# Performance work log

Hardware: AMD Instinct MI355X
Metric: run time of the kernel (lower is better)

## Reference

```python
import jax, jax.numpy as jnp
import numpy as np

T, B, H = 512, 32, 512   # seq, batch, hidden_dim (hidden has 2*H channels)
D = 512                  # label_dim
V = 32000                # vocab
L = 2048                 # number of labels (spans)
K = 2                    # tags per label (regularized ragged tags)


def setup_inputs() -> dict:
    key = jax.random.key(0)
    ks = jax.random.split(key, 11)
    hidden = jax.random.normal(ks[0], (T, B, 2 * H), dtype=jnp.float32)
    begins = jax.random.randint(ks[1], (L,), 1, T - 1)   # begin-1 >= 0
    ends = jax.random.randint(ks[2], (L,), 1, T - 1)     # end <= T-1, end-1 >= 0
    bids = jax.random.randint(ks[3], (L,), 0, B)
    tags = jax.random.randint(ks[4], (L, K), 0, V)
    s = 1.0 / np.sqrt(2 * H)
    Wc = jax.random.uniform(ks[5], (D, 2 * H), minval=-s, maxval=s, dtype=jnp.float32)
    bc = jax.random.uniform(ks[6], (D,), minval=-s, maxval=s, dtype=jnp.float32)
    Wp = jax.random.uniform(ks[7], (D, 2 * H), minval=-s, maxval=s, dtype=jnp.float32)
    bp = jax.random.uniform(ks[8], (D,), minval=-s, maxval=s, dtype=jnp.float32)
    s2 = 1.0 / np.sqrt(D)
    Wo = jax.random.uniform(ks[9], (V, D), minval=-s2, maxval=s2, dtype=jnp.float32)
    bo = jnp.zeros((V,), jnp.float32)
    # discard probs per SoftmaxLoss._discard_probs from synthetic counts
    counts = jax.random.uniform(ks[10], (V,), minval=0.5, maxval=100.0, dtype=jnp.float32)
    freqs = counts / counts.sum()
    discard_probs = jnp.maximum(1.0 - jnp.sqrt(1e-4 / freqs), 0.0)
    return dict(hidden=hidden, Wc=Wc, bc=bc, Wp=Wp, bp=bp, Wo=Wo, bo=bo,
                discard_probs=discard_probs, begins=begins, ends=ends,
                bids=bids, tags=tags)


def reference(hidden, Wc, bc, Wp, bp, Wo, bo, discard_probs,
              begins, ends, bids, tags):
    Hd = hidden.shape[-1] // 2
    # span gathers (vectorized over all labels)
    h_bm1 = hidden[begins - 1, bids]                 # [L, 2H]
    h_end = hidden[ends, bids]                       # [L, 2H]
    context = jnp.concatenate([h_bm1[:, :Hd], h_end[:, Hd:]], axis=-1)  # [L, 2H]
    phrase = (hidden[begins, bids] + hidden[ends - 1, bids]) * 0.5      # [L, 2H]
    # FFNs (dropout = identity in eval mode)
    cf = jnp.tanh(context @ Wc.T + bc)               # [L, D]
    pf = jnp.tanh(phrase @ Wp.T + bp)                # [L, D]
    feats = jnp.concatenate([cf, pf], axis=0)        # [2L, D]
    # softmax loss with discard-prob scaling
    logsm = jax.nn.log_softmax(feats @ Wo.T + bo, axis=-1)  # [2L, V]
    tg = jnp.concatenate([tags, tags], axis=0)       # [2L, K]
    neg = -jnp.take_along_axis(logsm, tg, axis=-1)   # [2L, K]
    ratio = 1.0 - discard_probs[tg]                  # [2L, K]
    loss_rows = (neg * ratio).sum(-1) / ratio.sum(-1)  # [2L]
    n = tg.shape[0]
    return (loss_rows.sum() / (n + 1e-5)).reshape(1)
```

## Files before the change

kernel.cpp:

```cpp
#include <hip/hip_runtime.h>
#include <stdint.h>

typedef uint16_t u16;
typedef uint8_t  u8;
typedef __bf16 bf16x8 __attribute__((ext_vector_type(8)));
typedef float f32x4 __attribute__((ext_vector_type(4)));
typedef int i32x4 __attribute__((ext_vector_type(4)));
typedef int i32x8 __attribute__((ext_vector_type(8)));

#define NSC    16
#define NTILES 250
#define NPART  (2 * NSC)
#define NROWS  4096

__device__ __forceinline__ u16 f2b(float x) {
    uint32_t u = __float_as_uint(x);
    u += 0x7FFF + ((u >> 16) & 1);
    return (u16)(u >> 16);
}

__device__ __forceinline__ u8 f32_to_fp8(float x) {
    uint32_t sign = (__float_as_uint(x) >> 24) & 0x80;
    float ax = fminf(fabsf(x), 448.f);
    uint32_t r;
    if (ax < 0.015625f) {
        r = (uint32_t)(int)rintf(ax * 512.f);
    } else {
        uint32_t u = __float_as_uint(ax);
        u += 0x0007FFFF + ((u >> 20) & 1);
        r = (((u >> 23) - 120) << 3) | ((u >> 20) & 7);
    }
    return (u8)(sign | r);
}

__device__ __forceinline__ float fp8_val(int b) {
    int e = (b >> 3) & 0xF, m = b & 7;
    float v = e ? __uint_as_float((uint32_t)(((e + 120) << 23) | (m << 20)))
                : (float)m * 0.001953125f;
    return (b & 0x80) ? -v : v;
}

__device__ __forceinline__ void cp16(const void* g, void* l) {
    __builtin_amdgcn_global_load_lds(
        (const __attribute__((address_space(1))) uint32_t*)g,
        (__attribute__((address_space(3))) uint32_t*)l, 16, 0, 0);
}

__device__ __forceinline__ float fast_tanh(float x) {
    x = fminf(15.f, fmaxf(-15.f, x));
    float e = __expf(2.f * x);
    return (e - 1.f) / (e + 1.f);
}

__global__ void k_convert8(const float* __restrict__ src, u8* __restrict__ dst, int n) {
    int i = (blockIdx.x * blockDim.x + threadIdx.x) * 4;
    int stride = gridDim.x * blockDim.x * 4;
    for (; i < n; i += stride) {
        float4 v = *(const float4*)(src + i);
        u8 o[4] = {f32_to_fp8(v.x * 32.f), f32_to_fp8(v.y * 32.f),
                   f32_to_fp8(v.z * 32.f), f32_to_fp8(v.w * 32.f)};
        *(uint32_t*)(dst + i) = *(const uint32_t*)o;
    }
}

__global__ void k_prep(const float* __restrict__ Wc, const float* __restrict__ Wp,
                       const float* __restrict__ hidden, const int* __restrict__ begins,
                       const int* __restrict__ ends, const int* __restrict__ bids,
                       u16* __restrict__ Wc_b, u16* __restrict__ Wp_b,
                       u16* __restrict__ ctx, u16* __restrict__ phr) {
    int b = blockIdx.x;
    if (b < 256) {
        int i = b * 2048 + threadIdx.x * 8;
        float4 a0 = *(const float4*)(Wc + i), a1 = *(const float4*)(Wc + i + 4);
        float4 p0 = *(const float4*)(Wp + i), p1 = *(const float4*)(Wp + i + 4);
        u16 oc[8] = {f2b(a0.x), f2b(a0.y), f2b(a0.z), f2b(a0.w),
                     f2b(a1.x), f2b(a1.y), f2b(a1.z), f2b(a1.w)};
        u16 op[8] = {f2b(p0.x), f2b(p0.y), f2b(p0.z), f2b(p0.w),
                     f2b(p1.x), f2b(p1.y), f2b(p1.z), f2b(p1.w)};
        *(int4*)(Wc_b + i) = *(const int4*)oc;
        *(int4*)(Wp_b + i) = *(const int4*)op;
        return;
    }
    int l = b - 256;
    int bg = begins[l], e = ends[l], bd = bids[l];
    const float* h_bm1 = hidden + ((size_t)(bg - 1) * 32 + bd) * 1024;
    const float* h_e   = hidden + ((size_t)e * 32 + bd) * 1024;
    const float* h_b   = hidden + ((size_t)bg * 32 + bd) * 1024;
    const float* h_em1 = hidden + ((size_t)(e - 1) * 32 + bd) * 1024;
    int d = threadIdx.x * 4;
    float4 c4 = (d < 512) ? *(const float4*)(h_bm1 + d) : *(const float4*)(h_e + d);
    float4 b4 = *(const float4*)(h_b + d);
    float4 e4 = *(const float4*)(h_em1 + d);
    u16 co[4] = {f2b(c4.x), f2b(c4.y), f2b(c4.z), f2b(c4.w)};
    u16 po[4] = {f2b(0.5f * (b4.x + e4.x)), f2b(0.5f * (b4.y + e4.y)),
                 f2b(0.5f * (b4.z + e4.z)), f2b(0.5f * (b4.w + e4.w))};
    *(uint64_t*)(ctx + (size_t)l * 1024 + d) = *(const uint64_t*)co;
    *(uint64_t*)(phr + (size_t)l * 1024 + d) = *(const uint64_t*)po;
}

__global__ __launch_bounds__(256) void k_feats(const u16* __restrict__ ctx, const u16* __restrict__ phr,
        const u16* __restrict__ Wc, const u16* __restrict__ Wp,
        const float* __restrict__ bc, const float* __restrict__ bp,
        u8* __restrict__ feats) {
    __shared__ __align__(16) u16 lA[64 * 32];
    __shared__ __align__(16) u16 lB[64 * 32];
    int z = blockIdx.z;
    const u16* A = z ? phr : ctx;
    const u16* W = z ? Wp : Wc;
    const float* bias = z ? bp : bc;
    int m0 = blockIdx.x * 64;
    int n0 = blockIdx.y * 64;
    int t = threadIdx.x;
    int lane = t & 63, w = t >> 6;
    int lrow = lane & 15, lq = lane >> 4;
    f32x4 zero = {0.f, 0.f, 0.f, 0.f};
    f32x4 acc[4];
    for (int i = 0; i < 4; i++) acc[i] = zero;
    int row = t >> 2, kseg = (t & 3) * 8;
    for (int kt = 0; kt < 32; kt++) {
        int k0 = kt * 32;
        __syncthreads();
        cp16(&A[(size_t)(m0 + row) * 1024 + k0 + kseg], &lA[t * 8]);
        cp16(&W[(size_t)(n0 + row) * 1024 + k0 + kseg], &lB[t * 8]);
        __syncthreads();
        bf16x8 af = *(bf16x8*)&lA[(w * 16 + lrow) * 32 + lq * 8];
        for (int ns = 0; ns < 4; ns++) {
            bf16x8 bfr = *(bf16x8*)&lB[(ns * 16 + lrow) * 32 + lq * 8];
            acc[ns] = __builtin_amdgcn_mfma_f32_16x16x32_bf16(af, bfr, acc[ns], 0, 0, 0);
        }
    }
    int zbase = z * 2048;
    for (int ns = 0; ns < 4; ns++) {
        int col = n0 + ns * 16 + lrow;
        float bv = bias[col];
        for (int r = 0; r < 4; r++) {
            int orow = zbase + m0 + w * 16 + lq * 4 + r;
            feats[(size_t)orow * 512 + col] = f32_to_fp8(16.f * fast_tanh(acc[ns][r] + bv));
        }
    }
}

__global__ __launch_bounds__(256, 2) void k_lse(const u8* __restrict__ feats,
        const u8* __restrict__ Wo, const float* __restrict__ bo, float* __restrict__ ps) {
    __shared__ __align__(16) u8 lds[4][128 * 128];
    int m0 = blockIdx.x * 128;
    int sc = blockIdx.y;
    int ts = (NTILES * sc) / NSC, te = (NTILES * (sc + 1)) / NSC;
    int t = threadIdx.x;
    int lane = t & 63, w = t >> 6;
    int lrow = lane & 15, lq = lane >> 4;
    int wrow = (w & 1) * 64, wcol = (w >> 1) * 64;
    int xm = lrow & 7;
    int xoA = ((2 * lq) ^ xm) * 16;
    int xoB = ((2 * lq + 1) ^ xm) * 16;

    int srow = t >> 3;
    int kb = ((t & 7) ^ ((t >> 3) & 7)) * 16;

    i32x8 af[4][4];
#pragma unroll
    for (int mi = 0; mi < 4; mi++)
#pragma unroll
        for (int kc = 0; kc < 4; kc++) {
            const u8* pa = feats + (size_t)(m0 + wrow + mi * 16 + lrow) * 512
                         + kc * 128 + lq * 32;
            i32x4 lo = *(const i32x4*)pa;
            i32x4 hi = *(const i32x4*)(pa + 16);
            af[mi][kc] = __builtin_shufflevector(lo, hi, 0, 1, 2, 3, 4, 5, 6, 7);
        }

    auto stageB = [&](int slot, int gr) {
        const u8* pB = Wo + (size_t)((gr >> 2) * 128 + srow) * 512 + (gr & 3) * 128 + kb;
        for (int j = 0; j < 4; j++)
            cp16(pB + (size_t)(32 * j) * 512, &lds[slot][t * 16 + j * 4096]);
    };

    float s_state[4][4];
    for (int mi = 0; mi < 4; mi++)
        for (int r = 0; r < 4; r++) s_state[mi][r] = 0.f;
    f32x4 zero = {0.f, 0.f, 0.f, 0.f};
    f32x4 acc[4][4];
    const float inv512 = 1.f / 512.f;

    int gr0 = ts * 4;
    stageB(0, gr0);
    stageB(1, gr0 + 1);
    stageB(2, gr0 + 2);

    for (int tile = ts; tile < te; ++tile) {
        int grt = tile * 4;
        bool notlast = (tile + 1 < te);
#pragma unroll
        for (int mi = 0; mi < 4; mi++)
#pragma unroll
            for (int ni = 0; ni < 4; ni++) acc[mi][ni] = zero;
#pragma unroll
        for (int kc = 0; kc < 4; kc++) {
            if (notlast || kc < 2)
                asm volatile("s_waitcnt vmcnt(8)" ::: "memory");
            else if (kc == 2)
                asm volatile("s_waitcnt vmcnt(4)" ::: "memory");
            else
                asm volatile("s_waitcnt vmcnt(0)" ::: "memory");
            __builtin_amdgcn_s_barrier();
            if (notlast || kc == 0)
                stageB((kc + 3) & 3, grt + kc + 3);
            const u8* bufB = lds[kc];
            __builtin_amdgcn_s_setprio(1);
#pragma unroll
            for (int ni = 0; ni < 4; ni++) {
                const u8* pb = bufB + (wcol + ni * 16 + lrow) * 128;
                i32x4 blo = *(const i32x4*)(pb + xoA);
                i32x4 bhi = *(const i32x4*)(pb + xoB);
                i32x8 bfr = __builtin_shufflevector(blo, bhi, 0, 1, 2, 3, 4, 5, 6, 7);
#pragma unroll
                for (int mi = 0; mi < 4; mi++)
                    acc[mi][ni] = __builtin_amdgcn_mfma_scale_f32_16x16x128_f8f6f4(
                        af[mi][kc], bfr, acc[mi][ni], 0, 0,
                        0, 0x7F7F7F7F, 0, 0x7F7F7F7F);
            }
            __builtin_amdgcn_s_setprio(0);
        }
        int n0 = tile * 128;
#pragma unroll
        for (int ni = 0; ni < 4; ni++) {
            float bv = bo[n0 + wcol + ni * 16 + lrow];
#pragma unroll
            for (int mi = 0; mi < 4; mi++)
#pragma unroll
                for (int r = 0; r < 4; r++)
                    s_state[mi][r] += __expf(fmaf(acc[mi][ni][r], inv512, bv));
        }
    }
    for (int mi = 0; mi < 4; mi++)
    for (int r = 0; r < 4; r++) {
        float s = s_state[mi][r];
        for (int off = 1; off < 16; off <<= 1) s += __shfl_xor(s, off);
        if (lrow == 0) {
            int row = m0 + wrow + mi * 16 + lq * 4 + r;
            ps[row * NPART + sc * 2 + (w >> 1)] = s;
        }
    }
}

__global__ void k_taglog(const u8* __restrict__ feats, const u8* __restrict__ Wo,
        const float* __restrict__ bo, const int* __restrict__ tags, float* __restrict__ tlog) {
    int i = blockIdx.x * 4 + (threadIdx.x >> 6);
    int lane = threadIdx.x & 63;
    int t0 = tags[(i & 2047) * 2 + 0];
    int t1 = tags[(i & 2047) * 2 + 1];
    uint64_t fa = *(const uint64_t*)(feats + (size_t)i * 512 + lane * 8);
    uint64_t wa = *(const uint64_t*)(Wo + (size_t)t0 * 512 + lane * 8);
    uint64_t wb = *(const uint64_t*)(Wo + (size_t)t1 * 512 + lane * 8);
    float s0 = 0.f, s1 = 0.f;
    for (int j = 0; j < 8; j++) {
        float fv = fp8_val((int)((fa >> (8 * j)) & 0xFF));
        s0 += fv * fp8_val((int)((wa >> (8 * j)) & 0xFF));
        s1 += fv * fp8_val((int)((wb >> (8 * j)) & 0xFF));
    }
    for (int off = 32; off >= 1; off >>= 1) {
        s0 += __shfl_down(s0, off);
        s1 += __shfl_down(s1, off);
    }
    if (lane == 0) {
        tlog[i * 2 + 0] = s0 * (1.f / 512.f) + bo[t0];
        tlog[i * 2 + 1] = s1 * (1.f / 512.f) + bo[t1];
    }
}

__global__ void k_final(const float* __restrict__ ps,
        const float* __restrict__ tlog, const int* __restrict__ tags,
        const float* __restrict__ dp, float* __restrict__ out) {
    __shared__ float red[256];
    int i = blockIdx.x * 256 + threadIdx.x;
    float S = 0.f;
    for (int j = 0; j < NPART; j++) S += ps[i * NPART + j];
    float lse = logf(S);
    float num = 0.f, den = 0.f;
    for (int k = 0; k < 2; k++) {
        int tg = tags[(i & 2047) * 2 + k];
        float r = 1.0f - dp[tg];
        num += r * (lse - tlog[i * 2 + k]);
        den += r;
    }
    red[threadIdx.x] = num / den;
    __syncthreads();
    for (int s = 128; s > 0; s >>= 1) {
        if (threadIdx.x < s) red[threadIdx.x] += red[threadIdx.x + s];
        __syncthreads();
    }
    if (threadIdx.x == 0) atomicAdd(out, red[0] / (4096.0f + 1e-5f));
}

extern "C" void kernel_launch(void* const* d_in, const int* in_sizes, int n_in,
                              void* d_out, int out_size, void* d_ws, size_t ws_size,
                              hipStream_t stream) {
    const float* hidden = (const float*)d_in[0];
    const float* Wc     = (const float*)d_in[1];
    const float* bc     = (const float*)d_in[2];
    const float* Wp     = (const float*)d_in[3];
    const float* bp     = (const float*)d_in[4];
    const float* Wo     = (const float*)d_in[5];
    const float* bo     = (const float*)d_in[6];
    const float* dp     = (const float*)d_in[7];
    const int* begins   = (const int*)d_in[8];
    const int* ends     = (const int*)d_in[9];
    const int* bids     = (const int*)d_in[10];
    const int* tags     = (const int*)d_in[11];
    float* out = (float*)d_out;

    u8*  Wo8     = (u8*)d_ws;
    u16* Wc_b    = (u16*)((char*)d_ws + 16384000);
    u16* Wp_b    = Wc_b + 524288;
    u16* ctx_b   = Wp_b + 524288;
    u16* phr_b   = ctx_b + 2097152;
    u8*  feats8  = (u8*)(phr_b + 2097152);
    float* ps    = (float*)ctx_b;
    float* tlog  = ps + NROWS * NPART;

    k_convert8<<<2048, 256, 0, stream>>>(Wo, Wo8, 16384000);
    k_prep<<<2304, 256, 0, stream>>>(Wc, Wp, hidden, begins, ends, bids,
                                     Wc_b, Wp_b, ctx_b, phr_b);
    k_feats<<<dim3(32, 8, 2), 256, 0, stream>>>(ctx_b, phr_b, Wc_b, Wp_b, bc, bp, feats8);
    k_lse<<<dim3(32, NSC), 256, 0, stream>>>(feats8, Wo8, bo, ps);
    k_taglog<<<1024, 256, 0, stream>>>(feats8, Wo8, bo, tags, tlog);
    hipMemsetAsync(d_out, 0, sizeof(float), stream);
    k_final<<<16, 256, 0, stream>>>(ps, tlog, tags, dp, out);
}
```

Baseline: 279.0 us.

## Restructure LSE kernel to 8 waves each owning 16 rows across all columns

The LSE GEMM block grows from 4 to 8 waves (512 threads). Each wave now computes a 16-row strip across all 128 columns of the tile, instead of a 64x64 quadrant. This cuts per-wave accumulator and A-fragment registers and halves per-thread staging loads, aiming for higher occupancy and latency hiding. The cost is that each B fragment read from LDS feeds only one MFMA instead of four, so LDS read traffic per MFMA rises. The partial-sum layout drops from 2*NSC to NSC per row to match.

Result: slower. 782.3 us (+180.4%).

```diff
diff --git a/kernel.cpp b/kernel.cpp
--- a/kernel.cpp
+++ b/kernel.cpp
@@ -10,7 +10,7 @@
 
 #define NSC    16
 #define NTILES 250
-#define NPART  (2 * NSC)
+#define NPART  NSC
 #define NROWS  4096
 
 __device__ __forceinline__ u16 f2b(float x) {
@@ -140,7 +140,7 @@
     }
 }
 
-__global__ __launch_bounds__(256, 2) void k_lse(const u8* __restrict__ feats,
+__global__ __launch_bounds__(512, 4) void k_lse(const u8* __restrict__ feats,
         const u8* __restrict__ Wo, const float* __restrict__ bo, float* __restrict__ ps) {
     __shared__ __align__(16) u8 lds[4][128 * 128];
     int m0 = blockIdx.x * 128;
@@ -149,7 +149,6 @@
     int t = threadIdx.x;
     int lane = t & 63, w = t >> 6;
     int lrow = lane & 15, lq = lane >> 4;
-    int wrow = (w & 1) * 64, wcol = (w >> 1) * 64;
     int xm = lrow & 7;
     int xoA = ((2 * lq) ^ xm) * 16;
     int xoB = ((2 * lq + 1) ^ xm) * 16;
@@ -157,29 +156,26 @@
     int srow = t >> 3;
     int kb = ((t & 7) ^ ((t >> 3) & 7)) * 16;
 
-    i32x8 af[4][4];
-#pragma unroll
-    for (int mi = 0; mi < 4; mi++)
+    i32x8 af[4];
+    {
+        const u8* pa = feats + (size_t)(m0 + w * 16 + lrow) * 512 + lq * 32;
 #pragma unroll
         for (int kc = 0; kc < 4; kc++) {
-            const u8* pa = feats + (size_t)(m0 + wrow + mi * 16 + lrow) * 512
-                         + kc * 128 + lq * 32;
-            i32x4 lo = *(const i32x4*)pa;
-            i32x4 hi = *(const i32x4*)(pa + 16);
-            af[mi][kc] = __builtin_shufflevector(lo, hi, 0, 1, 2, 3, 4, 5, 6, 7);
-        }
+            i32x4 lo = *(const i32x4*)(pa + kc * 128);
+            i32x4 hi = *(const i32x4*)(pa + kc * 128 + 16);
+            af[kc] = __builtin_shufflevector(lo, hi, 0, 1, 2, 3, 4, 5, 6, 7);
+        }
+    }
 
     auto stageB = [&](int slot, int gr) {
         const u8* pB = Wo + (size_t)((gr >> 2) * 128 + srow) * 512 + (gr & 3) * 128 + kb;
-        for (int j = 0; j < 4; j++)
-            cp16(pB + (size_t)(32 * j) * 512, &lds[slot][t * 16 + j * 4096]);
+        cp16(pB, &lds[slot][t * 16]);
+        cp16(pB + (size_t)64 * 512, &lds[slot][t * 16 + 8192]);
     };
 
-    float s_state[4][4];
-    for (int mi = 0; mi < 4; mi++)
-        for (int r = 0; r < 4; r++) s_state[mi][r] = 0.f;
+    float s_state[4] = {0.f, 0.f, 0.f, 0.f};
     f32x4 zero = {0.f, 0.f, 0.f, 0.f};
-    f32x4 acc[4][4];
+    f32x4 acc[8];
     const float inv512 = 1.f / 512.f;
 
     int gr0 = ts * 4;
@@ -191,15 +187,13 @@
         int grt = tile * 4;
         bool notlast = (tile + 1 < te);
 #pragma unroll
-        for (int mi = 0; mi < 4; mi++)
-#pragma unroll
-            for (int ni = 0; ni < 4; ni++) acc[mi][ni] = zero;
+        for (int ni = 0; ni < 8; ni++) acc[ni] = zero;
 #pragma unroll
         for (int kc = 0; kc < 4; kc++) {
             if (notlast || kc < 2)
-                asm volatile("s_waitcnt vmcnt(8)" ::: "memory");
+                asm volatile("s_waitcnt vmcnt(4)" ::: "memory");
             else if (kc == 2)
-                asm volatile("s_waitcnt vmcnt(4)" ::: "memory");
+                asm volatile("s_waitcnt vmcnt(2)" ::: "memory");
             else
                 asm volatile("s_waitcnt vmcnt(0)" ::: "memory");
             __builtin_amdgcn_s_barrier();
@@ -208,37 +202,32 @@
             const u8* bufB = lds[kc];
             __builtin_amdgcn_s_setprio(1);
 #pragma unroll
-            for (int ni = 0; ni < 4; ni++) {
-                const u8* pb = bufB + (wcol + ni * 16 + lrow) * 128;
+            for (int ni = 0; ni < 8; ni++) {
+                const u8* pb = bufB + (ni * 16 + lrow) * 128;
                 i32x4 blo = *(const i32x4*)(pb + xoA);
                 i32x4 bhi = *(const i32x4*)(pb + xoB);
                 i32x8 bfr = __builtin_shufflevector(blo, bhi, 0, 1, 2, 3, 4, 5, 6, 7);
-#pragma unroll
-                for (int mi = 0; mi < 4; mi++)
-                    acc[mi][ni] = __builtin_amdgcn_mfma_scale_f32_16x16x128_f8f6f4(
-                        af[mi][kc], bfr, acc[mi][ni], 0, 0,
-                        0, 0x7F7F7F7F, 0, 0x7F7F7F7F);
+                acc[ni] = __builtin_amdgcn_mfma_scale_f32_16x16x128_f8f6f4(
+                    af[kc], bfr, acc[ni], 0, 0,
+                    0, 0x7F7F7F7F, 0, 0x7F7F7F7F);
             }
             __builtin_amdgcn_s_setprio(0);
         }
         int n0 = tile * 128;
 #pragma unroll
-        for (int ni = 0; ni < 4; ni++) {
-            float bv = bo[n0 + wcol + ni * 16 + lrow];
-#pragma unroll
-            for (int mi = 0; mi < 4; mi++)
-#pragma unroll
-                for (int r = 0; r < 4; r++)
-                    s_state[mi][r] += __expf(fmaf(acc[mi][ni][r], inv512, bv));
-        }
-    }
-    for (int mi = 0; mi < 4; mi++)
+        for (int ni = 0; ni < 8; ni++) {
+            float bv = bo[n0 + ni * 16 + lrow];
+#pragma unroll
+            for (int r = 0; r < 4; r++)
+                s_state[r] += __expf(fmaf(acc[ni][r], inv512, bv));
+        }
+    }
     for (int r = 0; r < 4; r++) {
-        float s = s_state[mi][r];
+        float s = s_state[r];
         for (int off = 1; off < 16; off <<= 1) s += __shfl_xor(s, off);
         if (lrow == 0) {
-            int row = m0 + wrow + mi * 16 + lq * 4 + r;
-            ps[row * NPART + sc * 2 + (w >> 1)] = s;
+            int row = m0 + w * 16 + lq * 4 + r;
+            ps[row * NPART + sc] = s;
         }
     }
 }
@@ -322,7 +311,7 @@
     k_prep<<<2304, 256, 0, stream>>>(Wc, Wp, hidden, begins, ends, bids,
                                      Wc_b, Wp_b, ctx_b, phr_b);
     k_feats<<<dim3(32, 8, 2), 256, 0, stream>>>(ctx_b, phr_b, Wc_b, Wp_b, bc, bp, feats8);
-    k_lse<<<dim3(32, NSC), 256, 0, stream>>>(feats8, Wo8, bo, ps);
+    k_lse<<<dim3(32, NSC), 512, 0, stream>>>(feats8, Wo8, bo, ps);
     k_taglog<<<1024, 256, 0, stream>>>(feats8, Wo8, bo, tags, tlog);
     hipMemsetAsync(d_out, 0, sizeof(float), stream);
     k_final<<<16, 256, 0, stream>>>(ps, tlog, tags, dp, out);
```

## Fuse Wo fp8 conversion into prep kernel and widen LSE blocks to 512 threads

Applied to the files above, without the earlier changes.

Folds the Wo fp32-to-fp8 conversion into the k_prep launch as extra blocks, removing one kernel launch. Reworks k_lse to use 512-thread blocks with 8 waves, each covering a 64x32 output slice instead of 64x64. This halves the per-wave accumulators, halves the per-thread staging copies, and halves the number of vocab splits (NSC 16 to 8) while keeping 32 partial sums per row. The A-fragment loads now start after the first B stages are issued so the two overlap. The trade-off is fewer blocks in the grid (256 instead of 512) at one block per CU, and each wave still loads the full A fragments, so A-operand reuse per wave drops.

Measured after the change: 270.4 us. -3.1%, faster.

```diff
diff --git a/kernel.cpp b/kernel.cpp
--- a/kernel.cpp
+++ b/kernel.cpp
@@ -8,9 +8,9 @@
 typedef int i32x4 __attribute__((ext_vector_type(4)));
 typedef int i32x8 __attribute__((ext_vector_type(8)));
 
-#define NSC    16
+#define NSC    8
 #define NTILES 250
-#define NPART  (2 * NSC)
+#define NPART  32
 #define NROWS  4096
 
 __device__ __forceinline__ u16 f2b(float x) {
@@ -52,23 +52,24 @@
     return (e - 1.f) / (e + 1.f);
 }
 
-__global__ void k_convert8(const float* __restrict__ src, u8* __restrict__ dst, int n) {
-    int i = (blockIdx.x * blockDim.x + threadIdx.x) * 4;
-    int stride = gridDim.x * blockDim.x * 4;
-    for (; i < n; i += stride) {
-        float4 v = *(const float4*)(src + i);
-        u8 o[4] = {f32_to_fp8(v.x * 32.f), f32_to_fp8(v.y * 32.f),
-                   f32_to_fp8(v.z * 32.f), f32_to_fp8(v.w * 32.f)};
-        *(uint32_t*)(dst + i) = *(const uint32_t*)o;
-    }
-}
-
 __global__ void k_prep(const float* __restrict__ Wc, const float* __restrict__ Wp,
                        const float* __restrict__ hidden, const int* __restrict__ begins,
                        const int* __restrict__ ends, const int* __restrict__ bids,
+                       const float* __restrict__ Wo, u8* __restrict__ Wo8,
                        u16* __restrict__ Wc_b, u16* __restrict__ Wp_b,
                        u16* __restrict__ ctx, u16* __restrict__ phr) {
     int b = blockIdx.x;
+    if (b >= 2304) {
+        int i = ((b - 2304) * 256 + threadIdx.x) * 4;
+        const int stride = 2048 * 256 * 4;
+        for (; i < 16384000; i += stride) {
+            float4 v = *(const float4*)(Wo + i);
+            u8 o[4] = {f32_to_fp8(v.x * 32.f), f32_to_fp8(v.y * 32.f),
+                       f32_to_fp8(v.z * 32.f), f32_to_fp8(v.w * 32.f)};
+            *(uint32_t*)(Wo8 + i) = *(const uint32_t*)o;
+        }
+        return;
+    }
     if (b < 256) {
         int i = b * 2048 + threadIdx.x * 8;
         float4 a0 = *(const float4*)(Wc + i), a1 = *(const float4*)(Wc + i + 4);
@@ -140,7 +141,7 @@
     }
 }
 
-__global__ __launch_bounds__(256, 2) void k_lse(const u8* __restrict__ feats,
+__global__ __launch_bounds__(512, 1) void k_lse(const u8* __restrict__ feats,
         const u8* __restrict__ Wo, const float* __restrict__ bo, float* __restrict__ ps) {
     __shared__ __align__(16) u8 lds[4][128 * 128];
     int m0 = blockIdx.x * 128;
@@ -149,7 +150,7 @@
     int t = threadIdx.x;
     int lane = t & 63, w = t >> 6;
     int lrow = lane & 15, lq = lane >> 4;
-    int wrow = (w & 1) * 64, wcol = (w >> 1) * 64;
+    int wrow = (w & 1) * 64, wcol = (w >> 1) * 32;
     int xm = lrow & 7;
     int xoA = ((2 * lq) ^ xm) * 16;
     int xoB = ((2 * lq + 1) ^ xm) * 16;
@@ -157,35 +158,35 @@
     int srow = t >> 3;
     int kb = ((t & 7) ^ ((t >> 3) & 7)) * 16;
 
-    i32x8 af[4][4];
-#pragma unroll
-    for (int mi = 0; mi < 4; mi++)
-#pragma unroll
-        for (int kc = 0; kc < 4; kc++) {
-            const u8* pa = feats + (size_t)(m0 + wrow + mi * 16 + lrow) * 512
-                         + kc * 128 + lq * 32;
-            i32x4 lo = *(const i32x4*)pa;
-            i32x4 hi = *(const i32x4*)(pa + 16);
-            af[mi][kc] = __builtin_shufflevector(lo, hi, 0, 1, 2, 3, 4, 5, 6, 7);
-        }
-
     auto stageB = [&](int slot, int gr) {
         const u8* pB = Wo + (size_t)((gr >> 2) * 128 + srow) * 512 + (gr & 3) * 128 + kb;
-        for (int j = 0; j < 4; j++)
-            cp16(pB + (size_t)(32 * j) * 512, &lds[slot][t * 16 + j * 4096]);
+        cp16(pB, &lds[slot][t * 16]);
+        cp16(pB + (size_t)64 * 512, &lds[slot][t * 16 + 8192]);
     };
+
+    int gr0 = ts * 4;
+    stageB(0, gr0);
+    stageB(1, gr0 + 1);
+    stageB(2, gr0 + 2);
+
+    i32x8 af[4][4];
+#pragma unroll
+    for (int mi = 0; mi < 4; mi++) {
+        const u8* pa = feats + (size_t)(m0 + wrow + mi * 16 + lrow) * 512 + lq * 32;
+#pragma unroll
+        for (int kc = 0; kc < 4; kc++) {
+            i32x4 lo = *(const i32x4*)(pa + kc * 128);
+            i32x4 hi = *(const i32x4*)(pa + kc * 128 + 16);
+            af[mi][kc] = __builtin_shufflevector(lo, hi, 0, 1, 2, 3, 4, 5, 6, 7);
+        }
+    }
 
     float s_state[4][4];
     for (int mi = 0; mi < 4; mi++)
         for (int r = 0; r < 4; r++) s_state[mi][r] = 0.f;
     f32x4 zero = {0.f, 0.f, 0.f, 0.f};
-    f32x4 acc[4][4];
+    f32x4 acc[4][2];
     const float inv512 = 1.f / 512.f;
-
-    int gr0 = ts * 4;
-    stageB(0, gr0);
-    stageB(1, gr0 + 1);
-    stageB(2, gr0 + 2);
 
     for (int tile = ts; tile < te; ++tile) {
         int grt = tile * 4;
@@ -193,13 +194,13 @@
 #pragma unroll
         for (int mi = 0; mi < 4; mi++)
 #pragma unroll
-            for (int ni = 0; ni < 4; ni++) acc[mi][ni] = zero;
+            for (int ni = 0; ni < 2; ni++) acc[mi][ni] = zero;
 #pragma unroll
         for (int kc = 0; kc < 4; kc++) {
             if (notlast || kc < 2)
-                asm volatile("s_waitcnt vmcnt(8)" ::: "memory");
+                asm volatile("s_waitcnt vmcnt(4)" ::: "memory");
             else if (kc == 2)
-                asm volatile("s_waitcnt vmcnt(4)" ::: "memory");
+                asm volatile("s_waitcnt vmcnt(2)" ::: "memory");
             else
                 asm volatile("s_waitcnt vmcnt(0)" ::: "memory");
             __builtin_amdgcn_s_barrier();
@@ -208,7 +209,7 @@
             const u8* bufB = lds[kc];
             __builtin_amdgcn_s_setprio(1);
 #pragma unroll
-            for (int ni = 0; ni < 4; ni++) {
+            for (int ni = 0; ni < 2; ni++) {
                 const u8* pb = bufB + (wcol + ni * 16 + lrow) * 128;
                 i32x4 blo = *(const i32x4*)(pb + xoA);
                 i32x4 bhi = *(const i32x4*)(pb + xoB);
@@ -223,7 +224,7 @@
         }
         int n0 = tile * 128;
 #pragma unroll
-        for (int ni = 0; ni < 4; ni++) {
+        for (int ni = 0; ni < 2; ni++) {
             float bv = bo[n0 + wcol + ni * 16 + lrow];
 #pragma unroll
             for (int mi = 0; mi < 4; mi++)
@@ -238,7 +239,7 @@
         for (int off = 1; off < 16; off <<= 1) s += __shfl_xor(s, off);
         if (lrow == 0) {
             int row = m0 + wrow + mi * 16 + lq * 4 + r;
-            ps[row * NPART + sc * 2 + (w >> 1)] = s;
+            ps[row * NPART + sc * 4 + (w >> 1)] = s;
         }
     }
 }
@@ -318,11 +319,10 @@
     float* ps    = (float*)ctx_b;
     float* tlog  = ps + NROWS * NPART;
 
-    k_convert8<<<2048, 256, 0, stream>>>(Wo, Wo8, 16384000);
-    k_prep<<<2304, 256, 0, stream>>>(Wc, Wp, hidden, begins, ends, bids,
-                                     Wc_b, Wp_b, ctx_b, phr_b);
+    k_prep<<<4352, 256, 0, stream>>>(Wc, Wp, hidden, begins, ends, bids,
+                                     Wo, Wo8, Wc_b, Wp_b, ctx_b, phr_b);
     k_feats<<<dim3(32, 8, 2), 256, 0, stream>>>(ctx_b, phr_b, Wc_b, Wp_b, bc, bp, feats8);
-    k_lse<<<dim3(32, NSC), 256, 0, stream>>>(feats8, Wo8, bo, ps);
+    k_lse<<<dim3(32, NSC), 512, 0, stream>>>(feats8, Wo8, bo, ps);
     k_taglog<<<1024, 256, 0, stream>>>(feats8, Wo8, bo, tags, tlog);
     hipMemsetAsync(d_out, 0, sizeof(float), stream);
     k_final<<<16, 256, 0, stream>>>(ps, tlog, tags, dp, out);
```
